# Kernel optimization log

Hardware: AMD Instinct MI355X
Metric: run time of the kernel (lower is better)

The kernel has to match this reference:

```python
import jax, jax.numpy as jnp
import numpy as np

P = 4        # number of GPU partitions (hardcoded in source)
N = 65536    # nodes per partition (src = dst for diagonal blocks)
D = 128      # in_d
O = 128      # out
E = 500000   # edges per (src, dest) block
M = 32768    # unique remote dest nodes per off-diagonal block


def setup_inputs() -> dict:
    key = jax.random.key(0)
    k0, k1, k2, k3, k4, k5 = jax.random.split(key, 6)
    feats = jax.random.normal(k0, (P, N, D), dtype=jnp.float32)
    scale = np.float32(1.0 / np.sqrt(D))
    W_self = jax.random.normal(k1, (P, D, O), dtype=jnp.float32) * scale
    W_neigh = jax.random.normal(k2, (P, D, O), dtype=jnp.float32) * scale
    b = jnp.zeros((P, O), dtype=jnp.float32)
    edge_src = jax.random.randint(k3, (P, P, E), 0, N, dtype=jnp.int32)
    # dest indices: < N on the diagonal, < M off-diagonal
    dst_max = np.where(np.eye(P, dtype=bool), N, M).astype(np.int32)  # [P,P]
    edge_dst = jax.random.randint(k4, (P, P, E), 0, N, dtype=jnp.int32) % jnp.asarray(dst_max)[:, :, None]
    # unique merge indices per off-diagonal block (diagonal entries unused)
    merge_idx = jnp.stack([
        jnp.stack([
            jax.random.permutation(jax.random.fold_in(k5, s * P + d), N)[:M].astype(jnp.int32)
            for d in range(P)])
        for s in range(P)])  # [P,P,M]
    return {"feats": feats, "W_self": W_self, "W_neigh": W_neigh, "b": b,
            "edge_src": edge_src, "edge_dst": edge_dst, "merge_idx": merge_idx}


def _sage_block(feat_src, Ws, Wn, bias, e_src, e_dst, num_dst):
    # DGL SAGEConv, aggregator='mean', norm=None, bipartite block:
    #   h_neigh[v] = mean_{(u,v) in E} feat_src[u]   (0 if in-degree 0)
    #   out = feat_dst @ W_self + h_neigh @ W_neigh + b, feat_dst = feat_src[:num_dst]
    msg = feat_src[e_src]                                              # [E, D] gather
    agg = jax.ops.segment_sum(msg, e_dst, num_segments=num_dst)        # [num_dst, D]
    deg = jax.ops.segment_sum(jnp.ones((e_src.shape[0],), feat_src.dtype),
                              e_dst, num_segments=num_dst)
    h_neigh = agg / jnp.maximum(deg, 1.0)[:, None]
    return feat_src[:num_dst] @ Ws + h_neigh @ Wn + bias


def reference(feats, W_self, W_neigh, b, edge_src, edge_dst, merge_idx):
    # per-(src,dest) SAGEConv using src partition's layer weights
    outs = [[_sage_block(feats[s], W_self[s], W_neigh[s], b[s],
                         edge_src[s, d], edge_dst[s, d],
                         N if s == d else M)
             for d in range(P)] for s in range(P)]
    # cross-partition merge: final[merge_idx] += remote partial
    finals = []
    for d in range(P):
        f = outs[d][d]                                                 # [N, O]
        for s in range(P):
            if s != d:
                f = f.at[merge_idx[s, d]].add(outs[s][d])              # scatter-add [M,O]
        finals.append(f)
    return jnp.stack(finals)                                           # [P, N, O]
```

## Files before the change

kernel.cpp:

```cpp
#include <hip/hip_runtime.h>
#include <stdint.h>

#define PN 4
#define NN 65536
#define DD 128
#define OO 128
#define EE 500000
#define MM 32768
#define NW 245

typedef __attribute__((ext_vector_type(8))) short short8;
typedef __attribute__((ext_vector_type(4))) float floatx4;
typedef __attribute__((ext_vector_type(4))) float f4v;
typedef __attribute__((ext_vector_type(2))) unsigned u2v;

__device__ __forceinline__ unsigned short f2bf(float f) {
  unsigned u = __float_as_uint(f);
  u += 0x7fffu + ((u >> 16) & 1u);
  return (unsigned short)(u >> 16);
}
__device__ __forceinline__ float bfhi2f(unsigned u) { return __uint_as_float(u & 0xffff0000u); }
__device__ __forceinline__ float bflo2f(unsigned u) { return __uint_as_float(u << 16); }

__device__ __forceinline__ long rowbase(int b) {
  int diagb = (b + 4) / 5;
  int offb = b - diagb;
  return (long)diagb * NN + (long)offb * MM;
}

__global__ __launch_bounds__(256) void cvt_kernel(const float* __restrict__ f,
                                                  unsigned short* __restrict__ o) {
  size_t i = (size_t)blockIdx.x * blockDim.x + threadIdx.x;
  f4v v = __builtin_nontemporal_load((const f4v*)f + i);
  uint2 r;
  r.x = ((unsigned)f2bf(v[1]) << 16) | f2bf(v[0]);
  r.y = ((unsigned)f2bf(v[3]) << 16) | f2bf(v[2]);
  ((uint2*)o)[i] = r;
}

__global__ __launch_bounds__(256) void packW_kernel(const float* __restrict__ Ws,
                                                    const float* __restrict__ Wn,
                                                    unsigned short* __restrict__ Wp) {
  int i = blockIdx.x * 256 + threadIdx.x;
  int k = i & 127;
  int col = (i >> 7) & 127;
  int s = (i >> 14) & 3;
  int mat = i >> 16;
  const float* W = mat ? Wn : Ws;
  Wp[i] = f2bf(W[((size_t)s * DD + k) * OO + col]);
}

__global__ __launch_bounds__(256) void bucket_count(const int* __restrict__ edst,
                                                    int* __restrict__ mat) {
  __shared__ int hist[256];
  int b = blockIdx.y, w = blockIdx.x, t = threadIdx.x;
  hist[t] = 0;
  __syncthreads();
  size_t ebase = (size_t)b * EE;
#pragma unroll
  for (int k = 0; k < 8; ++k) {
    int e = w * 2048 + k * 256 + t;
    if (e < EE) atomicAdd(&hist[edst[ebase + e] >> 8], 1);
  }
  __syncthreads();
  mat[((size_t)b * NW + w) * 256 + t] = hist[t];
}

__global__ __launch_bounds__(256) void bucket_colscan(int* __restrict__ mat,
                                                      int* __restrict__ btot) {
  int t = threadIdx.x;
  int wid = blockIdx.x * 4 + (t >> 6);
  int l = t & 63;
  int b = wid >> 8, beta = wid & 255;
  int run = 0;
  for (int c = 0; c < 4; ++c) {
    int w = c * 64 + l;
    size_t idx = ((size_t)b * NW + w) * 256 + beta;
    int v = (w < NW) ? mat[idx] : 0;
    int x = v;
#pragma unroll
    for (int off = 1; off < 64; off <<= 1) {
      int y = __shfl_up(x, off);
      if (l >= off) x += y;
    }
    if (w < NW) mat[idx] = run + x - v;
    run += __shfl(x, 63);
  }
  if (l == 0) btot[b * 256 + beta] = run;
}

__global__ __launch_bounds__(256) void bucket_base(const int* __restrict__ btot,
                                                   int* __restrict__ bbase) {
  __shared__ int sc[256];
  int b = blockIdx.x, t = threadIdx.x;
  int v = btot[b * 256 + t];
  sc[t] = v;
  __syncthreads();
  for (int off = 1; off < 256; off <<= 1) {
    int x = (t >= off) ? sc[t - off] : 0;
    __syncthreads();
    sc[t] += x;
    __syncthreads();
  }
  bbase[b * 256 + t] = sc[t] - v;
}

__global__ __launch_bounds__(256) void bucket_scatter(const int* __restrict__ esrc,
                                                      const int* __restrict__ edst,
                                                      const int* __restrict__ mat,
                                                      const int* __restrict__ bbase,
                                                      uint2* __restrict__ tmp) {
  __shared__ int cur[256];
  int b = blockIdx.y, w = blockIdx.x, t = threadIdx.x;
  cur[t] = bbase[b * 256 + t] + mat[((size_t)b * NW + w) * 256 + t];
  __syncthreads();
  size_t ebase = (size_t)b * EE;
#pragma unroll
  for (int k = 0; k < 8; ++k) {
    int e = w * 2048 + k * 256 + t;
    if (e < EE) {
      int dv = __builtin_nontemporal_load(&edst[ebase + e]);
      int sv = __builtin_nontemporal_load(&esrc[ebase + e]);
      int p = atomicAdd(&cur[dv >> 8], 1);
      tmp[ebase + p] = (uint2){(unsigned)dv, (unsigned)sv};
    }
  }
}

__global__ __launch_bounds__(256) void csr_build(const uint2* __restrict__ tmp,
                                                 const int* __restrict__ btot,
                                                 const int* __restrict__ bbase,
                                                 int* __restrict__ deg,
                                                 int* __restrict__ offs,
                                                 int* __restrict__ csr) {
  __shared__ int hist[256], sc[256], cur[256];
  int b = blockIdx.y, beta = blockIdx.x, t = threadIdx.x;
  int cnt = btot[b * 256 + beta];
  int segbase = bbase[b * 256 + beta];
  hist[t] = 0;
  __syncthreads();
  size_t tbase = (size_t)b * EE + segbase;
  for (int i = t; i < cnt; i += 256) atomicAdd(&hist[tmp[tbase + i].x & 255], 1);
  __syncthreads();
  sc[t] = hist[t];
  __syncthreads();
  for (int off = 1; off < 256; off <<= 1) {
    int x = (t >= off) ? sc[t - off] : 0;
    __syncthreads();
    sc[t] += x;
    __syncthreads();
  }
  int excl = sc[t] - hist[t];
  int v = beta * 256 + t;
  deg[b * NN + v] = hist[t];
  offs[b * NN + v] = segbase + excl;
  cur[t] = excl;
  __syncthreads();
  const u2v* tp = (const u2v*)tmp;
  for (int i = t; i < cnt; i += 256) {
    u2v pr = __builtin_nontemporal_load(tp + tbase + i);
    int p = atomicAdd(&cur[pr[0] & 255], 1);
    csr[(size_t)b * EE + segbase + p] = (int)pr[1];
  }
}

__global__ __launch_bounds__(256) void agg_kernel(const unsigned short* __restrict__ featsbf,
                                                  const int* __restrict__ csr,
                                                  const int* __restrict__ offs,
                                                  const int* __restrict__ deg,
                                                  unsigned short* __restrict__ hbuf) {
  int b = blockIdx.y;
  int s = b >> 2, d = b & 3;
  int num_dst = (s == d) ? NN : MM;
  int v = blockIdx.x * 4 + (threadIdx.x >> 6);
  if (v >= num_dst) return;
  int l = threadIdx.x & 63;
  const unsigned* F = (const unsigned*)(featsbf + (size_t)s * NN * DD);
  int o  = __builtin_amdgcn_readfirstlane(offs[b * NN + v]);
  int dg = __builtin_amdgcn_readfirstlane(deg[b * NN + v]);
  const int* cs = csr + (size_t)b * EE + o;

  float alo[4] = {0.f, 0.f, 0.f, 0.f};
  float ahi[4] = {0.f, 0.f, 0.f, 0.f};

  for (int base = 0; base < dg; base += 64) {
    int rem = dg - base;
    int cnt = rem < 64 ? rem : 64;
    int myidx = (l < cnt) ? __builtin_nontemporal_load(&cs[base + l]) : 0;
    int j = 0;
    for (; j + 8 <= cnt; j += 8) {
      unsigned p[8];
#pragma unroll
      for (int q = 0; q < 8; ++q) {
        int idx = __builtin_amdgcn_readlane(myidx, j + q);
        p[q] = F[(size_t)idx * 64 + l];
      }
#pragma unroll
      for (int q = 0; q < 8; ++q) { alo[q & 3] += bflo2f(p[q]); ahi[q & 3] += bfhi2f(p[q]); }
    }
    for (; j + 4 <= cnt; j += 4) {
      unsigned p[4];
#pragma unroll
      for (int q = 0; q < 4; ++q) {
        int idx = __builtin_amdgcn_readlane(myidx, j + q);
        p[q] = F[(size_t)idx * 64 + l];
      }
#pragma unroll
      for (int q = 0; q < 4; ++q) { alo[q] += bflo2f(p[q]); ahi[q] += bfhi2f(p[q]); }
    }
    for (; j < cnt; ++j) {
      int idx = __builtin_amdgcn_readlane(myidx, j);
      unsigned p = F[(size_t)idx * 64 + l];
      alo[0] += bflo2f(p); ahi[0] += bfhi2f(p);
    }
  }

  float a0 = (alo[0] + alo[1]) + (alo[2] + alo[3]);
  float a1 = (ahi[0] + ahi[1]) + (ahi[2] + ahi[3]);
  float inv = 1.0f / (float)(dg > 0 ? dg : 1);
  a0 *= inv; a1 *= inv;
  unsigned pk = ((unsigned)f2bf(a1) << 16) | f2bf(a0);
  __builtin_nontemporal_store(pk, &((unsigned*)hbuf)[(rowbase(b) + v) * 64 + l]);
}

__global__ __launch_bounds__(256) void gemm_kernel(const unsigned short* __restrict__ featsbf,
                                                   const unsigned short* __restrict__ hbuf,
                                                   const unsigned short* __restrict__ Wpack,
                                                   const float* __restrict__ bias,
                                                   const int* __restrict__ merge,
                                                   float* __restrict__ out,
                                                   int offdiag, int round) {
  int w = threadIdx.x >> 6;
  int l = threadIdx.x & 63;
  int s, d;
  if (!offdiag) { d = blockIdx.y; s = d; }
  else { s = blockIdx.y; d = (s + 1 + round) & 3; }
  int b = s * 4 + d;
  int row0 = blockIdx.x * 64;
  int kq = l >> 4;
  int m16 = l & 15;
  int n0 = w * 32;

  const unsigned short* Aself = featsbf + (size_t)s * NN * DD;
  const unsigned short* Ah = hbuf + (size_t)rowbase(b) * DD;

  short8 bfrag[2][4][2];
#pragma unroll
  for (int mat = 0; mat < 2; ++mat) {
    const unsigned short* WT = Wpack + ((size_t)(mat * PN + s) * OO) * DD;
#pragma unroll
    for (int kk = 0; kk < 4; ++kk) {
#pragma unroll
      for (int t = 0; t < 2; ++t) {
        int col = n0 + 16 * t + m16;
        bfrag[mat][kk][t] =
            *reinterpret_cast<const short8*>(WT + (size_t)col * DD + kk * 32 + kq * 8);
      }
    }
  }

  floatx4 acc[4][2];
#pragma unroll
  for (int rt = 0; rt < 4; ++rt)
#pragma unroll
    for (int t = 0; t < 2; ++t) acc[rt][t] = (floatx4){0.f, 0.f, 0.f, 0.f};

#pragma unroll
  for (int mat = 0; mat < 2; ++mat) {
    const unsigned short* A = mat ? Ah : Aself;
#pragma unroll
    for (int kk = 0; kk < 4; ++kk) {
#pragma unroll
      for (int rt = 0; rt < 4; ++rt) {
        int row = row0 + rt * 16 + m16;
        short8 af = *reinterpret_cast<const short8*>(A + (size_t)row * DD + kk * 32 + kq * 8);
        acc[rt][0] = __builtin_amdgcn_mfma_f32_16x16x32_bf16(af, bfrag[mat][kk][0], acc[rt][0], 0, 0, 0);
        acc[rt][1] = __builtin_amdgcn_mfma_f32_16x16x32_bf16(af, bfrag[mat][kk][1], acc[rt][1], 0, 0, 0);
      }
    }
  }

  float bs0 = bias[s * OO + n0 + m16];
  float bs1 = bias[s * OO + n0 + 16 + m16];
  float* outd = out + (size_t)d * NN * OO;
  if (!offdiag) {
#pragma unroll
    for (int rt = 0; rt < 4; ++rt) {
#pragma unroll
      for (int r = 0; r < 4; ++r) {
        int row = row0 + rt * 16 + kq * 4 + r;
        outd[(size_t)row * OO + n0 + m16] = acc[rt][0][r] + bs0;
        outd[(size_t)row * OO + n0 + 16 + m16] = acc[rt][1][r] + bs1;
      }
    }
  } else {
    const int* mg = merge + ((size_t)s * PN + d) * MM;
#pragma unroll
    for (int rt = 0; rt < 4; ++rt) {
#pragma unroll
      for (int r = 0; r < 4; ++r) {
        int row = row0 + rt * 16 + kq * 4 + r;
        int u = mg[row];
        float* p0 = &outd[(size_t)u * OO + n0 + m16];
        float* p1 = &outd[(size_t)u * OO + n0 + 16 + m16];
        *p0 = *p0 + acc[rt][0][r] + bs0;
        *p1 = *p1 + acc[rt][1][r] + bs1;
      }
    }
  }
}

extern "C" void kernel_launch(void* const* d_in, const int* in_sizes, int n_in,
                              void* d_out, int out_size, void* d_ws, size_t ws_size,
                              hipStream_t stream) {
  const float* feats = (const float*)d_in[0];
  const float* Wself = (const float*)d_in[1];
  const float* Wneigh = (const float*)d_in[2];
  const float* bias = (const float*)d_in[3];
  const int* esrc = (const int*)d_in[4];
  const int* edst = (const int*)d_in[5];
  const int* merge = (const int*)d_in[6];
  float* out = (float*)d_out;

  char* ws = (char*)d_ws;
  unsigned short* featsbf = (unsigned short*)(ws);
  int* deg   = (int*)(ws + 67108864);
  int* offs  = (int*)(ws + 71303168);
  int* csr   = (int*)(ws + 75497472);
  unsigned short* hbuf = (unsigned short*)(ws + 107497472);
  unsigned short* Wpack = (unsigned short*)(ws + 275269632);
  int* btot  = (int*)(ws + 275531776);
  int* bbase = (int*)(ws + 275548160);
  uint2* tmp = (uint2*)(ws + 107497472);
  int* mat   = (int*)(ws + 107497472 + 64000000);

  cvt_kernel<<<(PN * NN * DD) / 4 / 256, 256, 0, stream>>>(feats, featsbf);
  packW_kernel<<<512, 256, 0, stream>>>(Wself, Wneigh, Wpack);
  bucket_count<<<dim3(NW, 16), 256, 0, stream>>>(edst, mat);
  bucket_colscan<<<1024, 256, 0, stream>>>(mat, btot);
  bucket_base<<<16, 256, 0, stream>>>(btot, bbase);
  bucket_scatter<<<dim3(NW, 16), 256, 0, stream>>>(esrc, edst, mat, bbase, tmp);
  csr_build<<<dim3(256, 16), 256, 0, stream>>>(tmp, btot, bbase, deg, offs, csr);
  agg_kernel<<<dim3(NN / 4, 16), 256, 0, stream>>>(featsbf, csr, offs, deg, hbuf);
  gemm_kernel<<<dim3(NN / 64, 4), 256, 0, stream>>>(featsbf, hbuf, Wpack, bias, merge, out, 0, 0);
  gemm_kernel<<<dim3(MM / 64, 4), 256, 0, stream>>>(featsbf, hbuf, Wpack, bias, merge, out, 1, 0);
  gemm_kernel<<<dim3(MM / 64, 4), 256, 0, stream>>>(featsbf, hbuf, Wpack, bias, merge, out, 1, 1);
  gemm_kernel<<<dim3(MM / 64, 4), 256, 0, stream>>>(featsbf, hbuf, Wpack, bias, merge, out, 1, 2);
}
```

Baseline: 1.041 ms.

## Fuse cross-partition merge into single GEMM via inverse merge index

Builds an inverse map from each destination node to its row in every off-diagonal block. One GEMM launch then accumulates the diagonal and all three remote partial products into registers per output tile and writes the output once. This removes three extra launches and the read-modify-write scatter passes over the fp32 output. The cost is gathered A-row loads (zeros when a node is absent) and MFMA work on every row of all four blocks, including rows with no remote contribution. It also drops the nontemporal hints in the aggregation kernel and reuses the CSR workspace region for the inverse map.

```diff
diff --git a/kernel.cpp b/kernel.cpp
--- a/kernel.cpp
+++ b/kernel.cpp
@@ -27,6 +27,7 @@
   int offb = b - diagb;
   return (long)diagb * NN + (long)offb * MM;
 }
+__device__ __forceinline__ int offidx(int b) { return b - (b + 4) / 5; }
 
 __global__ __launch_bounds__(256) void cvt_kernel(const float* __restrict__ f,
                                                   unsigned short* __restrict__ o) {
@@ -186,7 +187,7 @@
   for (int base = 0; base < dg; base += 64) {
     int rem = dg - base;
     int cnt = rem < 64 ? rem : 64;
-    int myidx = (l < cnt) ? __builtin_nontemporal_load(&cs[base + l]) : 0;
+    int myidx = (l < cnt) ? cs[base + l] : 0;
     int j = 0;
     for (; j + 8 <= cnt; j += 8) {
       unsigned p[8];
@@ -220,92 +221,138 @@
   float inv = 1.0f / (float)(dg > 0 ? dg : 1);
   a0 *= inv; a1 *= inv;
   unsigned pk = ((unsigned)f2bf(a1) << 16) | f2bf(a0);
-  __builtin_nontemporal_store(pk, &((unsigned*)hbuf)[(rowbase(b) + v) * 64 + l]);
+  ((unsigned*)hbuf)[(rowbase(b) + v) * 64 + l] = pk;
+}
+
+__global__ __launch_bounds__(256) void inv_zero(int* __restrict__ inv) {
+  inv[blockIdx.x * 256 + threadIdx.x] = 0;
+}
+__global__ __launch_bounds__(256) void inv_scatter(const int* __restrict__ merge,
+                                                   int* __restrict__ inv) {
+  int i = blockIdx.x * 256 + threadIdx.x;
+  int p = i >> 15;
+  int m = i & (MM - 1);
+  int s = p / 3;
+  int dd = p % 3;
+  int d = dd + (dd >= s ? 1 : 0);
+  int u = merge[((size_t)(s * PN + d)) * MM + m];
+  inv[p * NN + u] = m + 1;
 }
 
 __global__ __launch_bounds__(256) void gemm_kernel(const unsigned short* __restrict__ featsbf,
                                                    const unsigned short* __restrict__ hbuf,
                                                    const unsigned short* __restrict__ Wpack,
                                                    const float* __restrict__ bias,
-                                                   const int* __restrict__ merge,
-                                                   float* __restrict__ out,
-                                                   int offdiag, int round) {
+                                                   const int* __restrict__ inv,
+                                                   float* __restrict__ out) {
   int w = threadIdx.x >> 6;
   int l = threadIdx.x & 63;
-  int s, d;
-  if (!offdiag) { d = blockIdx.y; s = d; }
-  else { s = blockIdx.y; d = (s + 1 + round) & 3; }
-  int b = s * 4 + d;
+  int d = blockIdx.y;
   int row0 = blockIdx.x * 64;
   int kq = l >> 4;
   int m16 = l & 15;
   int n0 = w * 32;
 
-  const unsigned short* Aself = featsbf + (size_t)s * NN * DD;
-  const unsigned short* Ah = hbuf + (size_t)rowbase(b) * DD;
-
-  short8 bfrag[2][4][2];
-#pragma unroll
-  for (int mat = 0; mat < 2; ++mat) {
-    const unsigned short* WT = Wpack + ((size_t)(mat * PN + s) * OO) * DD;
-#pragma unroll
-    for (int kk = 0; kk < 4; ++kk) {
-#pragma unroll
-      for (int t = 0; t < 2; ++t) {
-        int col = n0 + 16 * t + m16;
-        bfrag[mat][kk][t] =
-            *reinterpret_cast<const short8*>(WT + (size_t)col * DD + kk * 32 + kq * 8);
+  floatx4 acc[4][2];
+#pragma unroll
+  for (int rt = 0; rt < 4; ++rt)
+#pragma unroll
+    for (int t = 0; t < 2; ++t) acc[rt][t] = (floatx4){0.f, 0.f, 0.f, 0.f};
+
+  {
+    int b = 5 * d;
+    const unsigned short* Aself = featsbf + (size_t)d * NN * DD;
+    const unsigned short* Ah = hbuf + (size_t)rowbase(b) * DD;
+    short8 bfrag[2][4][2];
+#pragma unroll
+    for (int mat = 0; mat < 2; ++mat) {
+      const unsigned short* WT = Wpack + ((size_t)(mat * PN + d) * OO) * DD;
+#pragma unroll
+      for (int kk = 0; kk < 4; ++kk)
+#pragma unroll
+        for (int t = 0; t < 2; ++t) {
+          int col = n0 + 16 * t + m16;
+          bfrag[mat][kk][t] =
+              *reinterpret_cast<const short8*>(WT + (size_t)col * DD + kk * 32 + kq * 8);
+        }
+    }
+#pragma unroll
+    for (int mat = 0; mat < 2; ++mat) {
+      const unsigned short* A = mat ? Ah : Aself;
+#pragma unroll
+      for (int kk = 0; kk < 4; ++kk)
+#pragma unroll
+        for (int rt = 0; rt < 4; ++rt) {
+          int row = row0 + rt * 16 + m16;
+          short8 af = *reinterpret_cast<const short8*>(A + (size_t)row * DD + kk * 32 + kq * 8);
+          acc[rt][0] = __builtin_amdgcn_mfma_f32_16x16x32_bf16(af, bfrag[mat][kk][0], acc[rt][0], 0, 0, 0);
+          acc[rt][1] = __builtin_amdgcn_mfma_f32_16x16x32_bf16(af, bfrag[mat][kk][1], acc[rt][1], 0, 0, 0);
+        }
+    }
+  }
+
+  int invj[3][4];
+  float bj0[3], bj1[3];
+#pragma unroll
+  for (int j = 0; j < 3; ++j) {
+    int s = j + (j >= d ? 1 : 0);
+    int b = s * 4 + d;
+    int p = offidx(b);
+    const int* invp = inv + (size_t)p * NN;
+#pragma unroll
+    for (int rt = 0; rt < 4; ++rt) invj[j][rt] = invp[row0 + rt * 16 + m16];
+    bj0[j] = bias[s * OO + n0 + m16];
+    bj1[j] = bias[s * OO + n0 + 16 + m16];
+
+    const unsigned short* As = featsbf + (size_t)s * NN * DD;
+    const unsigned short* Hs = hbuf + (size_t)rowbase(b) * DD;
+    short8 bfrag[2][4][2];
+#pragma unroll
+    for (int mat = 0; mat < 2; ++mat) {
+      const unsigned short* WT = Wpack + ((size_t)(mat * PN + s) * OO) * DD;
+#pragma unroll
+      for (int kk = 0; kk < 4; ++kk)
+#pragma unroll
+        for (int t = 0; t < 2; ++t) {
+          int col = n0 + 16 * t + m16;
+          bfrag[mat][kk][t] =
+              *reinterpret_cast<const short8*>(WT + (size_t)col * DD + kk * 32 + kq * 8);
+        }
+    }
+#pragma unroll
+    for (int mat = 0; mat < 2; ++mat) {
+      const unsigned short* A = mat ? Hs : As;
+#pragma unroll
+      for (int kk = 0; kk < 4; ++kk)
+#pragma unroll
+        for (int rt = 0; rt < 4; ++rt) {
+          int idx = invj[j][rt];
+          short8 af = (short8){0, 0, 0, 0, 0, 0, 0, 0};
+          if (idx > 0)
+            af = *reinterpret_cast<const short8*>(A + (size_t)(idx - 1) * DD + kk * 32 + kq * 8);
+          acc[rt][0] = __builtin_amdgcn_mfma_f32_16x16x32_bf16(af, bfrag[mat][kk][0], acc[rt][0], 0, 0, 0);
+          acc[rt][1] = __builtin_amdgcn_mfma_f32_16x16x32_bf16(af, bfrag[mat][kk][1], acc[rt][1], 0, 0, 0);
+        }
+    }
+  }
+
+  float bs0 = bias[d * OO + n0 + m16];
+  float bs1 = bias[d * OO + n0 + 16 + m16];
+  float* outd = out + (size_t)d * NN * OO;
+#pragma unroll
+  for (int rt = 0; rt < 4; ++rt) {
+#pragma unroll
+    for (int r = 0; r < 4; ++r) {
+      int row = row0 + rt * 16 + kq * 4 + r;
+      float v0 = acc[rt][0][r] + bs0;
+      float v1 = acc[rt][1][r] + bs1;
+#pragma unroll
+      for (int j = 0; j < 3; ++j) {
+        int iv = __shfl(invj[j][rt], kq * 4 + r);
+        if (iv > 0) { v0 += bj0[j]; v1 += bj1[j]; }
       }
-    }
-  }
-
-  floatx4 acc[4][2];
-#pragma unroll
-  for (int rt = 0; rt < 4; ++rt)
-#pragma unroll
-    for (int t = 0; t < 2; ++t) acc[rt][t] = (floatx4){0.f, 0.f, 0.f, 0.f};
-
-#pragma unroll
-  for (int mat = 0; mat < 2; ++mat) {
-    const unsigned short* A = mat ? Ah : Aself;
-#pragma unroll
-    for (int kk = 0; kk < 4; ++kk) {
-#pragma unroll
-      for (int rt = 0; rt < 4; ++rt) {
-        int row = row0 + rt * 16 + m16;
-        short8 af = *reinterpret_cast<const short8*>(A + (size_t)row * DD + kk * 32 + kq * 8);
-        acc[rt][0] = __builtin_amdgcn_mfma_f32_16x16x32_bf16(af, bfrag[mat][kk][0], acc[rt][0], 0, 0, 0);
-        acc[rt][1] = __builtin_amdgcn_mfma_f32_16x16x32_bf16(af, bfrag[mat][kk][1], acc[rt][1], 0, 0, 0);
-      }
-    }
-  }
-
-  float bs0 = bias[s * OO + n0 + m16];
-  float bs1 = bias[s * OO + n0 + 16 + m16];
-  float* outd = out + (size_t)d * NN * OO;
-  if (!offdiag) {
-#pragma unroll
-    for (int rt = 0; rt < 4; ++rt) {
-#pragma unroll
-      for (int r = 0; r < 4; ++r) {
-        int row = row0 + rt * 16 + kq * 4 + r;
-        outd[(size_t)row * OO + n0 + m16] = acc[rt][0][r] + bs0;
-        outd[(size_t)row * OO + n0 + 16 + m16] = acc[rt][1][r] + bs1;
-      }
-    }
-  } else {
-    const int* mg = merge + ((size_t)s * PN + d) * MM;
-#pragma unroll
-    for (int rt = 0; rt < 4; ++rt) {
-#pragma unroll
-      for (int r = 0; r < 4; ++r) {
-        int row = row0 + rt * 16 + kq * 4 + r;
-        int u = mg[row];
-        float* p0 = &outd[(size_t)u * OO + n0 + m16];
-        float* p1 = &outd[(size_t)u * OO + n0 + 16 + m16];
-        *p0 = *p0 + acc[rt][0][r] + bs0;
-        *p1 = *p1 + acc[rt][1][r] + bs1;
-      }
+      outd[(size_t)row * OO + n0 + m16] = v0;
+      outd[(size_t)row * OO + n0 + 16 + m16] = v1;
     }
   }
 }
@@ -333,6 +380,7 @@
   int* bbase = (int*)(ws + 275548160);
   uint2* tmp = (uint2*)(ws + 107497472);
   int* mat   = (int*)(ws + 107497472 + 64000000);
+  int* inv   = (int*)(ws + 75497472);
 
   cvt_kernel<<<(PN * NN * DD) / 4 / 256, 256, 0, stream>>>(feats, featsbf);
   packW_kernel<<<512, 256, 0, stream>>>(Wself, Wneigh, Wpack);
@@ -342,8 +390,7 @@
   bucket_scatter<<<dim3(NW, 16), 256, 0, stream>>>(esrc, edst, mat, bbase, tmp);
   csr_build<<<dim3(256, 16), 256, 0, stream>>>(tmp, btot, bbase, deg, offs, csr);
   agg_kernel<<<dim3(NN / 4, 16), 256, 0, stream>>>(featsbf, csr, offs, deg, hbuf);
-  gemm_kernel<<<dim3(NN / 64, 4), 256, 0, stream>>>(featsbf, hbuf, Wpack, bias, merge, out, 0, 0);
-  gemm_kernel<<<dim3(MM / 64, 4), 256, 0, stream>>>(featsbf, hbuf, Wpack, bias, merge, out, 1, 0);
-  gemm_kernel<<<dim3(MM / 64, 4), 256, 0, stream>>>(featsbf, hbuf, Wpack, bias, merge, out, 1, 1);
-  gemm_kernel<<<dim3(MM / 64, 4), 256, 0, stream>>>(featsbf, hbuf, Wpack, bias, merge, out, 1, 2);
-}
+  inv_zero<<<12 * NN / 256, 256, 0, stream>>>(inv);
+  inv_scatter<<<12 * MM / 256, 256, 0, stream>>>(merge, inv);
+  gemm_kernel<<<dim3(NN / 64, 4), 256, 0, stream>>>(featsbf, hbuf, Wpack, bias, inv, out);
+}
```

After: 1.101 ms. 1.06x slower.
